# Kernel tuning notes

Hardware: AMD Instinct MI355X
Metric: run time of the kernel (lower is better)

Reference implementation:

```python
import jax, jax.numpy as jnp
import numpy as np

TY = 10  # decoder loop uses the global Ty=10 in the original code


def _bi_lstm_dir(X, Wih, Whh, b, n_hidden):
    # X: (m, T, F); returns hidden states (m, T, n_hidden). Gate order: i,f,g,o.
    m = X.shape[0]
    def step(carry, x_t):
        h, c = carry
        g = x_t @ Wih.T + h @ Whh.T + b
        i, f, gg, o = jnp.split(g, 4, axis=-1)
        c = jax.nn.sigmoid(f) * c + jax.nn.sigmoid(i) * jnp.tanh(gg)
        h = jax.nn.sigmoid(o) * jnp.tanh(c)
        return (h, c), h
    h0 = jnp.zeros((m, n_hidden), X.dtype)
    _, hs = jax.lax.scan(step, (h0, h0), jnp.swapaxes(X, 0, 1))
    return jnp.swapaxes(hs, 0, 1)


def setup_inputs() -> dict:
    key = jax.random.key(0)
    ks = jax.random.split(key, 17)
    m, Tx, F = 256, 256, 128
    n_a, n_s, vocab, attn_h = 256, 512, 1024, 10
    def w(k, shape, fan_in):
        return (jax.random.normal(k, shape, jnp.float32) / np.sqrt(fan_in)).astype(jnp.float32)
    return {
        "X": jax.random.normal(ks[0], (m, Tx, F), jnp.float32),
        "Wih_f": w(ks[1], (4 * n_a, F), F),
        "Whh_f": w(ks[2], (4 * n_a, n_a), n_a),
        "b_f": w(ks[3], (4 * n_a,), n_a),
        "Wih_b": w(ks[4], (4 * n_a, F), F),
        "Whh_b": w(ks[5], (4 * n_a, n_a), n_a),
        "b_b": w(ks[6], (4 * n_a,), n_a),
        "W1": w(ks[7], (attn_h, 2 * n_a + n_s), 2 * n_a + n_s),
        "b1": w(ks[8], (attn_h,), attn_h),
        "W2": w(ks[9], (1, attn_h), attn_h),
        "b2": w(ks[10], (1,), attn_h),
        "Wc_ih": w(ks[11], (4 * n_s, n_s), n_s),
        "Wc_hh": w(ks[12], (4 * n_s, n_s), n_s),
        "bc": w(ks[13], (4 * n_s,), n_s),
        "Wfc": w(ks[14], (vocab, n_s), n_s),
        "bfc": w(ks[15], (vocab,), n_s),
    }


def reference(X, Wih_f, Whh_f, b_f, Wih_b, Whh_b, b_b, W1, b1, W2, b2, Wc_ih, Wc_hh, bc, Wfc, bfc):
    m, Tx, _ = X.shape
    n_a = Whh_f.shape[1]
    n_s = Wc_hh.shape[1]
    # bidirectional encoder
    a_f = _bi_lstm_dir(X, Wih_f, Whh_f, b_f, n_a)
    a_b = _bi_lstm_dir(X[:, ::-1], Wih_b, Whh_b, b_b, n_a)[:, ::-1]
    a = jnp.concatenate([a_f, a_b], axis=-1)  # (m, Tx, 2*n_a)
    # decoder: initial h_n = zeros(m, 2, n_a).flatten(1) == zeros(m, n_s) since n_s = 2*n_a
    s = jnp.zeros((m, n_s), X.dtype)
    c = jnp.zeros((m, n_s), X.dtype)
    outs = []
    for _ in range(TY):
        sp = jnp.broadcast_to(s[:, None, :], (m, Tx, n_s))
        concat = jnp.concatenate([a, sp], axis=-1)           # (m, Tx, 2*n_a + n_s)
        e = jnp.tanh(concat @ W1.T + b1)                     # (m, Tx, 10)
        scores = jax.nn.relu(e @ W2.T + b2)                  # (m, Tx, 1)
        alphas = jax.nn.softmax(scores, axis=1)              # softmax over Tx
        context = jnp.sum(alphas * a, axis=1)                # (m, 2*n_a) == (m, n_s)
        g = context @ Wc_ih.T + s @ Wc_hh.T + bc             # LSTMCell
        i, f, gg, o = jnp.split(g, 4, axis=-1)
        c = jax.nn.sigmoid(f) * c + jax.nn.sigmoid(i) * jnp.tanh(gg)
        s = jax.nn.sigmoid(o) * jnp.tanh(c)
        outs.append(s @ Wfc.T + bfc)                         # (m, vocab)
    return jnp.stack(outs, axis=1)                           # (m, Ty, vocab)
```

## Files before the change

kernel.cpp:

```cpp
#include <hip/hip_runtime.h>
#include <hip/hip_bf16.h>

#define TXN 256
#define NA 256
#define NF 128
#define NS 512
#define TYN 10
#define VOCAB 1024

#define A_STR 392
#define W_STR 392
#define WL_OFF (64 * W_STR)
#define AH_OFF (2 * 64 * W_STR)
#define AL_OFF (AH_OFF + 32 * A_STR)
#define PRE_OFF_US (AL_OFF + 32 * A_STR)
#define ENC_LDS_BYTES (150528 + 32 * 68 * 4 + 64 * 4)

#define D_STR 264
#define D_WH 0
#define D_WL (64 * D_STR)
#define D_AH (2 * 64 * D_STR)
#define D_AL (D_AH + 32 * D_STR)
#define D_PRE_US (D_AL + 32 * D_STR)
#define DEC_LDS_BYTES (101376 + 32 * 68 * 4 + 64 * 4)

typedef __attribute__((ext_vector_type(8))) short bf16x8;
typedef __attribute__((ext_vector_type(4))) float f32x4;

__device__ __forceinline__ float fsigmoid(float x) { return 1.f / (1.f + __expf(-x)); }
__device__ __forceinline__ float ftanh(float x)    { return 1.f - 2.f / (1.f + __expf(2.f * x)); }

__device__ __forceinline__ void split_bf16(float v, unsigned short& hi, unsigned short& lo) {
    __hip_bfloat16 h = __float2bfloat16(v);
    float rem = v - __bfloat162float(h);
    __hip_bfloat16 l = __float2bfloat16(rem);
    hi = *reinterpret_cast<unsigned short*>(&h);
    lo = *reinterpret_cast<unsigned short*>(&l);
}

__device__ __forceinline__ float agent_ld(const float* p) {
    return __hip_atomic_load(p, __ATOMIC_RELAXED, __HIP_MEMORY_SCOPE_AGENT);
}
__device__ __forceinline__ void agent_st(float* p, float v) {
    __hip_atomic_store(p, v, __ATOMIC_RELAXED, __HIP_MEMORY_SCOPE_AGENT);
}
__device__ __forceinline__ unsigned flag_ld(const unsigned* p) {
    return __hip_atomic_load(p, __ATOMIC_RELAXED, __HIP_MEMORY_SCOPE_AGENT);
}
__device__ __forceinline__ void flag_st(unsigned* p, unsigned v) {
    __hip_atomic_store(p, v, __ATOMIC_RELAXED, __HIP_MEMORY_SCOPE_AGENT);
}

__global__ __launch_bounds__(512, 1) void encoder_kernel(
    const float* __restrict__ X,
    const float* __restrict__ Wih_f, const float* __restrict__ Whh_f, const float* __restrict__ b_f,
    const float* __restrict__ Wih_b, const float* __restrict__ Whh_b, const float* __restrict__ b_b,
    float* __restrict__ a, unsigned int* __restrict__ bar)
{
    extern __shared__ unsigned char smem_raw[];
    unsigned short* Wh  = (unsigned short*)smem_raw;
    unsigned short* Wl  = (unsigned short*)smem_raw + WL_OFF;
    unsigned short* Ahh = (unsigned short*)smem_raw + AH_OFF;
    unsigned short* All = (unsigned short*)smem_raw + AL_OFF;
    float* Pre = (float*)(smem_raw + (size_t)PRE_OFF_US * 2);
    float* bsh = Pre + 32 * 68;

    const int tid = threadIdx.x;
    const int xcd = blockIdx.x & 7;
    const int sub = (blockIdx.x >> 3) & 1;
    const int jb  = blockIdx.x >> 4;
    const int dir = sub;
    const int ig  = xcd;
    const int i0 = ig * 32;
    const int j0 = jb * 16;
    const int grp = dir * 8 + ig;
    const int myjb = jb;
    unsigned int* slots = bar + grp * 16;

    const float* __restrict__ Wih = dir ? Wih_b : Wih_f;
    const float* __restrict__ Whh = dir ? Whh_b : Whh_f;
    const float* __restrict__ bv  = dir ? b_b  : b_f;

    if (tid < 64) bsh[tid] = bv[(tid >> 4) * NA + j0 + (tid & 15)];

    {
        const int col = tid & 255;
        const int r0w = (tid >> 8) * 32;
        for (int r = r0w; r < r0w + 32; ++r) {
            int row = (r >> 4) * NA + j0 + (r & 15);
            unsigned short hi, lo;
            split_bf16(Whh[(size_t)row * NA + col], hi, lo);
            Wh[r * W_STR + col] = hi;
            Wl[r * W_STR + col] = lo;
            if (col < NF) {
                split_bf16(Wih[(size_t)row * NF + col], hi, lo);
                Wh[r * W_STR + 256 + col] = hi;
                Wl[r * W_STR + 256 + col] = lo;
            }
        }
    }

    {
        const int col = tid & 255;
        const int r0z = (tid >> 8) * 16;
        #pragma unroll 4
        for (int r = r0z; r < r0z + 16; ++r) {
            Ahh[r * A_STR + col] = 0;
            All[r * A_STR + col] = 0;
        }
    }

    {
        const int t0 = dir ? (TXN - 1) : 0;
        const int kx = tid & 127;
        const int rbase = tid >> 7;
        #pragma unroll 4
        for (int rr = 0; rr < 8; ++rr) {
            int r = rr * 4 + rbase;
            float v = X[((size_t)(i0 + r) * TXN + t0) * NF + kx];
            unsigned short hi, lo;
            split_bf16(v, hi, lo);
            Ahh[r * A_STR + 256 + kx] = hi;
            All[r * A_STR + 256 + kx] = lo;
        }
    }
    __syncthreads();

    float cC = 0.f;
    const int jl  = tid & 15;
    const int epr = tid >> 4;

    const int lane = tid & 63;
    const int wv   = tid >> 6;
    const int rt   = wv >> 1;
    const int g0   = (wv & 1) * 2;
    const int ln   = lane & 15;
    const int quad = lane >> 4;
    const unsigned short* pAh = Ahh + (rt * 16 + ln) * A_STR + quad * 8;
    const unsigned short* pAl = All + (rt * 16 + ln) * A_STR + quad * 8;
    const unsigned short* pW0h = Wh + (g0 * 16 + ln) * W_STR + quad * 8;
    const unsigned short* pW0l = Wl + (g0 * 16 + ln) * W_STR + quad * 8;
    const unsigned short* pW1h = pW0h + 16 * W_STR;
    const unsigned short* pW1l = pW0l + 16 * W_STR;

    for (int step = 0; step < TXN; ++step) {
        const int t = dir ? (TXN - 1 - step) : step;

        f32x4 a0e = {0.f,0.f,0.f,0.f}, a0o = {0.f,0.f,0.f,0.f};
        f32x4 a1e = {0.f,0.f,0.f,0.f}, a1o = {0.f,0.f,0.f,0.f};

        if (tid < 256) {
            #pragma unroll
            for (int k4 = 0; k4 < 4; ++k4) {
                const int kc = 8 + k4;
                bf16x8 fah = *(const bf16x8*)(pAh + kc * 32);
                bf16x8 fal = *(const bf16x8*)(pAl + kc * 32);
                bf16x8 w0h = *(const bf16x8*)(pW0h + kc * 32);
                bf16x8 w0l = *(const bf16x8*)(pW0l + kc * 32);
                bf16x8 w1h = *(const bf16x8*)(pW1h + kc * 32);
                bf16x8 w1l = *(const bf16x8*)(pW1l + kc * 32);
                if ((kc & 1) == 0) {
                    a0e = __builtin_amdgcn_mfma_f32_16x16x32_bf16(fal, w0h, a0e, 0, 0, 0);
                    a0e = __builtin_amdgcn_mfma_f32_16x16x32_bf16(fah, w0l, a0e, 0, 0, 0);
                    a0e = __builtin_amdgcn_mfma_f32_16x16x32_bf16(fah, w0h, a0e, 0, 0, 0);
                    a1e = __builtin_amdgcn_mfma_f32_16x16x32_bf16(fal, w1h, a1e, 0, 0, 0);
                    a1e = __builtin_amdgcn_mfma_f32_16x16x32_bf16(fah, w1l, a1e, 0, 0, 0);
                    a1e = __builtin_amdgcn_mfma_f32_16x16x32_bf16(fah, w1h, a1e, 0, 0, 0);
                } else {
                    a0o = __builtin_amdgcn_mfma_f32_16x16x32_bf16(fal, w0h, a0o, 0, 0, 0);
                    a0o = __builtin_amdgcn_mfma_f32_16x16x32_bf16(fah, w0l, a0o, 0, 0, 0);
                    a0o = __builtin_amdgcn_mfma_f32_16x16x32_bf16(fah, w0h, a0o, 0, 0, 0);
                    a1o = __builtin_amdgcn_mfma_f32_16x16x32_bf16(fal, w1h, a1o, 0, 0, 0);
                    a1o = __builtin_amdgcn_mfma_f32_16x16x32_bf16(fah, w1l, a1o, 0, 0, 0);
                    a1o = __builtin_amdgcn_mfma_f32_16x16x32_bf16(fah, w1h, a1o, 0, 0, 0);
                }
            }
        } else if (step != 0) {
            const int tprev = dir ? (t + 1) : (t - 1);
            const int colh = tid & 255;
            const int jw = colh >> 4;
            while (flag_ld(&slots[jw]) < (unsigned)step) {}
            float hv[32];
            #pragma unroll
            for (int r = 0; r < 32; ++r) {
                hv[r] = agent_ld(&a[(((size_t)(i0 + r) * TXN + tprev) << 9) + dir * NA + colh]);
            }
            #pragma unroll
            for (int r = 0; r < 32; ++r) {
                unsigned short hi, lo;
                split_bf16(hv[r], hi, lo);
                Ahh[r * A_STR + colh] = hi;
                All[r * A_STR + colh] = lo;
            }
        }
        __syncthreads();

        if (tid < 256) {
            #pragma unroll
            for (int kp = 0; kp < 4; ++kp) {
                {
                    const int kc = kp * 2;
                    bf16x8 fah = *(const bf16x8*)(pAh + kc * 32);
                    bf16x8 fal = *(const bf16x8*)(pAl + kc * 32);
                    bf16x8 w0h = *(const bf16x8*)(pW0h + kc * 32);
                    bf16x8 w0l = *(const bf16x8*)(pW0l + kc * 32);
                    bf16x8 w1h = *(const bf16x8*)(pW1h + kc * 32);
                    bf16x8 w1l = *(const bf16x8*)(pW1l + kc * 32);
                    a0e = __builtin_amdgcn_mfma_f32_16x16x32_bf16(fal, w0h, a0e, 0, 0, 0);
                    a0e = __builtin_amdgcn_mfma_f32_16x16x32_bf16(fah, w0l, a0e, 0, 0, 0);
                    a0e = __builtin_amdgcn_mfma_f32_16x16x32_bf16(fah, w0h, a0e, 0, 0, 0);
                    a1e = __builtin_amdgcn_mfma_f32_16x16x32_bf16(fal, w1h, a1e, 0, 0, 0);
                    a1e = __builtin_amdgcn_mfma_f32_16x16x32_bf16(fah, w1l, a1e, 0, 0, 0);
                    a1e = __builtin_amdgcn_mfma_f32_16x16x32_bf16(fah, w1h, a1e, 0, 0, 0);
                }
                {
                    const int kc = kp * 2 + 1;
                    bf16x8 fah = *(const bf16x8*)(pAh + kc * 32);
                    bf16x8 fal = *(const bf16x8*)(pAl + kc * 32);
                    bf16x8 w0h = *(const bf16x8*)(pW0h + kc * 32);
                    bf16x8 w0l = *(const bf16x8*)(pW0l + kc * 32);
                    bf16x8 w1h = *(const bf16x8*)(pW1h + kc * 32);
                    bf16x8 w1l = *(const bf16x8*)(pW1l + kc * 32);
                    a0o = __builtin_amdgcn_mfma_f32_16x16x32_bf16(fal, w0h, a0o, 0, 0, 0);
                    a0o = __builtin_amdgcn_mfma_f32_16x16x32_bf16(fah, w0l, a0o, 0, 0, 0);
                    a0o = __builtin_amdgcn_mfma_f32_16x16x32_bf16(fah, w0h, a0o, 0, 0, 0);
                    a1o = __builtin_amdgcn_mfma_f32_16x16x32_bf16(fal, w1h, a1o, 0, 0, 0);
                    a1o = __builtin_amdgcn_mfma_f32_16x16x32_bf16(fah, w1l, a1o, 0, 0, 0);
                    a1o = __builtin_amdgcn_mfma_f32_16x16x32_bf16(fah, w1h, a1o, 0, 0, 0);
                }
            }
            #pragma unroll
            for (int reg = 0; reg < 4; ++reg) {
                int prow = rt * 16 + quad * 4 + reg;
                Pre[prow * 68 + g0 * 16 + ln]       = a0e[reg] + a0o[reg];
                Pre[prow * 68 + (g0 + 1) * 16 + ln] = a1e[reg] + a1o[reg];
            }
        }
        __syncthreads();

        {
            float gi = fsigmoid(Pre[epr * 68 +      jl] + bsh[jl]);
            float gf = fsigmoid(Pre[epr * 68 + 16 + jl] + bsh[16 + jl]);
            float gg = ftanh  (Pre[epr * 68 + 32 + jl] + bsh[32 + jl]);
            float go = fsigmoid(Pre[epr * 68 + 48 + jl] + bsh[48 + jl]);
            cC = gf * cC + gi * gg;
            float h = go * ftanh(cC);
            agent_st(&a[(((size_t)(i0 + epr) * TXN + t) << 9) + dir * NA + j0 + jl], h);
        }

        if (step != TXN - 1) {
            __syncthreads();
            if (tid == 0) flag_st(&slots[myjb], (unsigned)(step + 1));
            {
                const int tn = dir ? (t - 1) : (t + 1);
                const int kx = tid & 127;
                const int rbase = tid >> 7;
                #pragma unroll 4
                for (int rr = 0; rr < 8; ++rr) {
                    int r = rr * 4 + rbase;
                    float v = X[((size_t)(i0 + r) * TXN + tn) * NF + kx];
                    unsigned short hi, lo;
                    split_bf16(v, hi, lo);
                    Ahh[r * A_STR + 256 + kx] = hi;
                    All[r * A_STR + 256 + kx] = lo;
                }
            }
            __syncthreads();
        }
    }
}

__global__ __launch_bounds__(256) void wsplit_cat(
    const float* __restrict__ Wc_ih, const float* __restrict__ Wc_hh,
    unsigned short* __restrict__ Wh, unsigned short* __restrict__ Wl)
{
    int idx = blockIdx.x * 256 + threadIdx.x;
    int r = idx >> 10, k = idx & 1023;
    float v = (k < 512) ? Wc_ih[(size_t)r * 512 + k] : Wc_hh[(size_t)r * 512 + (k - 512)];
    unsigned short hi, lo;
    split_bf16(v, hi, lo);
    Wh[idx] = hi; Wl[idx] = lo;
}

__global__ __launch_bounds__(256) void wsplit_fc(
    const float* __restrict__ Wfc,
    unsigned short* __restrict__ Wh, unsigned short* __restrict__ Wl)
{
    int idx = blockIdx.x * 256 + threadIdx.x;
    unsigned short hi, lo;
    split_bf16(Wfc[idx], hi, lo);
    Wh[idx] = hi; Wl[idx] = lo;
}

__global__ __launch_bounds__(256) void attn_prep(
    const float* __restrict__ a, const float* __restrict__ W1,
    const float* __restrict__ b1, float* __restrict__ aW1)
{
    __shared__ float Wsh[10][516];
    __shared__ float red[64][10][4];
    const int tid = threadIdx.x;
    for (int idx = tid; idx < 10 * 512; idx += 256) {
        int o = idx >> 9, k = idx & 511;
        Wsh[o][k] = W1[o * 1024 + k];
    }
    __syncthreads();
    const int r = tid >> 2, kq = tid & 3;
    const float* ar = a + ((size_t)blockIdx.x * 64 + r) * 512 + kq * 128;
    float acc[10] = {};
    for (int k = 0; k < 128; k += 4) {
        float4 v = *(const float4*)&ar[k];
        #pragma unroll
        for (int o = 0; o < 10; ++o) {
            float4 w = *(const float4*)&Wsh[o][kq * 128 + k];
            acc[o] += v.x * w.x + v.y * w.y + v.z * w.z + v.w * w.w;
        }
    }
    #pragma unroll
    for (int o = 0; o < 10; ++o) red[r][o][kq] = acc[o];
    __syncthreads();
    for (int idx = tid; idx < 640; idx += 256) {
        int rr = idx / 10, o = idx % 10;
        float s = red[rr][o][0] + red[rr][o][1] + red[rr][o][2] + red[rr][o][3] + b1[o];
        aW1[((size_t)blockIdx.x * 64 + rr) * 10 + o] = s;
    }
}

__global__ __launch_bounds__(256) void attn_kernel(
    const float* __restrict__ aW1,
    const float* __restrict__ s_prev, int sp_stride,
    const float* __restrict__ W1,
    const float* __restrict__ W2,
    const float* __restrict__ b2,
    const float* __restrict__ a,
    float* __restrict__ xcat)
{
    __shared__ float sh_s[10];
    __shared__ float sh_w2[10];
    __shared__ float sred[160];
    __shared__ float red[256];
    __shared__ float al[256];
    __shared__ float4 ctxred[256];
    const int i = blockIdx.x;
    const int tid = threadIdx.x;

    if (tid < 160) {
        int o = tid >> 4, part = tid & 15;
        const float* srow = s_prev + (size_t)i * sp_stride;
        const float* wrow = W1 + o * 1024 + 512;
        float p = 0.f;
        for (int k = part; k < 512; k += 16) p += srow[k] * wrow[k];
        sred[tid] = p;
    }
    __syncthreads();
    if (tid < 10) {
        float v = 0.f;
        #pragma unroll
        for (int p = 0; p < 16; ++p) v += sred[tid * 16 + p];
        sh_s[tid] = v;
        sh_w2[tid] = W2[tid];
    }
    __syncthreads();

    float sum = b2[0];
    const float* ar = aW1 + ((size_t)i * TXN + tid) * 10;
    #pragma unroll
    for (int h = 0; h < 10; ++h) {
        float e = ftanh(ar[h] + sh_s[h]);
        sum += e * sh_w2[h];
    }
    float sc = fmaxf(sum, 0.f);

    red[tid] = sc;
    __syncthreads();
    for (int s = 128; s > 0; s >>= 1) {
        if (tid < s) red[tid] = fmaxf(red[tid], red[tid + s]);
        __syncthreads();
    }
    float mx = red[0];
    __syncthreads();
    float p = __expf(sc - mx);
    red[tid] = p;
    __syncthreads();
    for (int s = 128; s > 0; s >>= 1) {
        if (tid < s) red[tid] += red[tid + s];
        __syncthreads();
    }
    float inv = 1.f / red[0];
    al[tid] = p * inv;
    __syncthreads();

    const int half = tid >> 7;
    const int q    = tid & 127;
    const float* abase = a + (size_t)i * TXN * NS + q * 4;
    float4 acc = make_float4(0.f, 0.f, 0.f, 0.f);
    #pragma unroll 8
    for (int t = half; t < TXN; t += 2) {
        float w = al[t];
        float4 v = *(const float4*)&abase[(size_t)t * NS];
        acc.x += w * v.x; acc.y += w * v.y; acc.z += w * v.z; acc.w += w * v.w;
    }
    ctxred[tid] = acc;
    __syncthreads();
    if (tid < 128) {
        float4 e = ctxred[tid];
        float4 o = ctxred[tid + 128];
        float4 r4 = make_float4(e.x + o.x, e.y + o.y, e.z + o.z, e.w + o.w);
        *(float4*)&xcat[(size_t)i * 512 + tid * 4] = r4;
    }
}

__global__ __launch_bounds__(256, 1) void gates_kernel(
    const float* __restrict__ xcat,
    const float* __restrict__ s_prev, int sp_stride,
    const unsigned short* __restrict__ Wch,
    const unsigned short* __restrict__ Wcl,
    const float* __restrict__ bc,
    float* __restrict__ c_buf,
    float* __restrict__ s_out, int so_stride)
{
    extern __shared__ unsigned char smem_raw[];
    unsigned short* Wh = (unsigned short*)smem_raw + D_WH;
    unsigned short* Wl = (unsigned short*)smem_raw + D_WL;
    unsigned short* Ah = (unsigned short*)smem_raw + D_AH;
    unsigned short* Al = (unsigned short*)smem_raw + D_AL;
    float* Pre = (float*)(smem_raw + (size_t)D_PRE_US * 2);
    float* bsh = Pre + 32 * 68;

    const int tid = threadIdx.x;
    const int i0 = blockIdx.x * 32;
    const int j0 = blockIdx.y * 16;

    if (tid < 64) bsh[tid] = bc[(tid >> 4) * 512 + j0 + (tid & 15)];

    const int lane = tid & 63;
    const int wv   = tid >> 6;
    const int rt   = wv >> 1;
    const int g0   = (wv & 1) * 2;
    const int ln   = lane & 15;
    const int quad = lane >> 4;
    const unsigned short* pAh = Ah + (rt * 16 + ln) * D_STR + quad * 8;
    const unsigned short* pAl = Al + (rt * 16 + ln) * D_STR + quad * 8;
    const unsigned short* pW0h = Wh + (g0 * 16 + ln) * D_STR + quad * 8;
    const unsigned short* pW0l = Wl + (g0 * 16 + ln) * D_STR + quad * 8;
    const unsigned short* pW1h = pW0h + 16 * D_STR;
    const unsigned short* pW1l = pW0l + 16 * D_STR;

    const int rW = tid >> 2;
    const int qW = (tid & 3) * 64;
    const int rowg = (rW >> 4) * 512 + j0 + (rW & 15);

    f32x4 a0 = {0.f,0.f,0.f,0.f}, a1 = {0.f,0.f,0.f,0.f};

    for (int ch = 0; ch < 4; ++ch) {
        const int kc0 = ch * 256;
        __syncthreads();
        #pragma unroll 8
        for (int r = 0; r < 32; ++r) {
            float v;
            if (ch < 2) v = xcat[(size_t)(i0 + r) * 512 + kc0 + tid];
            else        v = s_prev[(size_t)(i0 + r) * sp_stride + (kc0 - 512) + tid];
            unsigned short hi, lo;
            split_bf16(v, hi, lo);
            Ah[r * D_STR + tid] = hi;
            Al[r * D_STR + tid] = lo;
        }
        {
            const size_t base = (size_t)rowg * 1024 + kc0 + qW;
            #pragma unroll
            for (int i = 0; i < 8; ++i) {
                *(bf16x8*)&Wh[rW * D_STR + qW + i * 8] = *(const bf16x8*)&Wch[base + i * 8];
                *(bf16x8*)&Wl[rW * D_STR + qW + i * 8] = *(const bf16x8*)&Wcl[base + i * 8];
            }
        }
        __syncthreads();
        #pragma unroll
        for (int kc = 0; kc < 8; ++kc) {
            bf16x8 fah = *(const bf16x8*)(pAh + kc * 32);
            bf16x8 fal = *(const bf16x8*)(pAl + kc * 32);
            bf16x8 w0h = *(const bf16x8*)(pW0h + kc * 32);
            bf16x8 w0l = *(const bf16x8*)(pW0l + kc * 32);
            bf16x8 w1h = *(const bf16x8*)(pW1h + kc * 32);
            bf16x8 w1l = *(const bf16x8*)(pW1l + kc * 32);
            a0 = __builtin_amdgcn_mfma_f32_16x16x32_bf16(fal, w0h, a0, 0, 0, 0);
            a0 = __builtin_amdgcn_mfma_f32_16x16x32_bf16(fah, w0l, a0, 0, 0, 0);
            a0 = __builtin_amdgcn_mfma_f32_16x16x32_bf16(fah, w0h, a0, 0, 0, 0);
            a1 = __builtin_amdgcn_mfma_f32_16x16x32_bf16(fal, w1h, a1, 0, 0, 0);
            a1 = __builtin_amdgcn_mfma_f32_16x16x32_bf16(fah, w1l, a1, 0, 0, 0);
            a1 = __builtin_amdgcn_mfma_f32_16x16x32_bf16(fah, w1h, a1, 0, 0, 0);
        }
    }
    __syncthreads();
    #pragma unroll
    for (int reg = 0; reg < 4; ++reg) {
        int prow = rt * 16 + quad * 4 + reg;
        Pre[prow * 68 + g0 * 16 + ln]       = a0[reg];
        Pre[prow * 68 + (g0 + 1) * 16 + ln] = a1[reg];
    }
    __syncthreads();

    const int jl = tid & 15;
    const int iA = (tid >> 4) * 2;
    #pragma unroll
    for (int rr = 0; rr < 2; ++rr) {
        int r = iA + rr;
        float gi = fsigmoid(Pre[r * 68 +      jl] + bsh[jl]);
        float gf = fsigmoid(Pre[r * 68 + 16 + jl] + bsh[16 + jl]);
        float gg = ftanh  (Pre[r * 68 + 32 + jl] + bsh[32 + jl]);
        float go = fsigmoid(Pre[r * 68 + 48 + jl] + bsh[48 + jl]);
        size_t ci = (size_t)(i0 + r) * 512 + j0 + jl;
        float cn = gf * c_buf[ci] + gi * gg;
        c_buf[ci] = cn;
        s_out[(size_t)(i0 + r) * so_stride + j0 + jl] = go * ftanh(cn);
    }
}

__global__ __launch_bounds__(256, 1) void logits_kernel(
    const float* __restrict__ S, int s_stride,
    const unsigned short* __restrict__ Wfh,
    const unsigned short* __restrict__ Wfl,
    const float* __restrict__ bfc,
    float* __restrict__ out, int o_stride, int o_off)
{
    extern __shared__ unsigned char smem_raw[];
    unsigned short* Wh = (unsigned short*)smem_raw + D_WH;
    unsigned short* Wl = (unsigned short*)smem_raw + D_WL;
    unsigned short* Ah = (unsigned short*)smem_raw + D_AH;
    unsigned short* Al = (unsigned short*)smem_raw + D_AL;

    const int tid = threadIdx.x;
    const int i0 = blockIdx.x * 32;
    const int v0 = blockIdx.y * 64;

    const int lane = tid & 63;
    const int wv   = tid >> 6;
    const int rt   = wv >> 1;
    const int ct   = wv & 1;
    const int ln   = lane & 15;
    const int quad = lane >> 4;
    const unsigned short* pAh = Ah + (rt * 16 + ln) * D_STR + quad * 8;
    const unsigned short* pAl = Al + (rt * 16 + ln) * D_STR + quad * 8;
    const unsigned short* pW0h = Wh + (ct * 32 + ln) * D_STR + quad * 8;
    const unsigned short* pW0l = Wl + (ct * 32 + ln) * D_STR + quad * 8;
    const unsigned short* pW1h = pW0h + 16 * D_STR;
    const unsigned short* pW1l = pW0l + 16 * D_STR;

    const int rW = tid >> 2;
    const int qW = (tid & 3) * 64;

    f32x4 a0 = {0.f,0.f,0.f,0.f}, a1 = {0.f,0.f,0.f,0.f};

    for (int ch = 0; ch < 2; ++ch) {
        const int kc0 = ch * 256;
        __syncthreads();
        #pragma unroll 8
        for (int r = 0; r < 32; ++r) {
            float v = S[(size_t)(i0 + r) * s_stride + kc0 + tid];
            unsigned short hi, lo;
            split_bf16(v, hi, lo);
            Ah[r * D_STR + tid] = hi;
            Al[r * D_STR + tid] = lo;
        }
        {
            const size_t base = (size_t)(v0 + rW) * 512 + kc0 + qW;
            #pragma unroll
            for (int i = 0; i < 8; ++i) {
                *(bf16x8*)&Wh[rW * D_STR + qW + i * 8] = *(const bf16x8*)&Wfh[base + i * 8];
                *(bf16x8*)&Wl[rW * D_STR + qW + i * 8] = *(const bf16x8*)&Wfl[base + i * 8];
            }
        }
        __syncthreads();
        #pragma unroll
        for (int kc = 0; kc < 8; ++kc) {
            bf16x8 fah = *(const bf16x8*)(pAh + kc * 32);
            bf16x8 fal = *(const bf16x8*)(pAl + kc * 32);
            bf16x8 w0h = *(const bf16x8*)(pW0h + kc * 32);
            bf16x8 w0l = *(const bf16x8*)(pW0l + kc * 32);
            bf16x8 w1h = *(const bf16x8*)(pW1h + kc * 32);
            bf16x8 w1l = *(const bf16x8*)(pW1l + kc * 32);
            a0 = __builtin_amdgcn_mfma_f32_16x16x32_bf16(fal, w0h, a0, 0, 0, 0);
            a0 = __builtin_amdgcn_mfma_f32_16x16x32_bf16(fah, w0l, a0, 0, 0, 0);
            a0 = __builtin_amdgcn_mfma_f32_16x16x32_bf16(fah, w0h, a0, 0, 0, 0);
            a1 = __builtin_amdgcn_mfma_f32_16x16x32_bf16(fal, w1h, a1, 0, 0, 0);
            a1 = __builtin_amdgcn_mfma_f32_16x16x32_bf16(fah, w1l, a1, 0, 0, 0);
            a1 = __builtin_amdgcn_mfma_f32_16x16x32_bf16(fah, w1h, a1, 0, 0, 0);
        }
    }
    #pragma unroll
    for (int reg = 0; reg < 4; ++reg) {
        int row = i0 + rt * 16 + quad * 4 + reg;
        int col0 = v0 + ct * 32 + ln;
        out[(size_t)row * o_stride + o_off + col0]      = a0[reg] + bfc[col0];
        out[(size_t)row * o_stride + o_off + col0 + 16] = a1[reg] + bfc[col0 + 16];
    }
}

extern "C" void kernel_launch(void* const* d_in, const int* in_sizes, int n_in,
                              void* d_out, int out_size, void* d_ws, size_t ws_size,
                              hipStream_t stream)
{
    const float* X     = (const float*)d_in[0];
    const float* Wih_f = (const float*)d_in[1];
    const float* Whh_f = (const float*)d_in[2];
    const float* b_f   = (const float*)d_in[3];
    const float* Wih_b = (const float*)d_in[4];
    const float* Whh_b = (const float*)d_in[5];
    const float* b_b   = (const float*)d_in[6];
    const float* W1    = (const float*)d_in[7];
    const float* b1    = (const float*)d_in[8];
    const float* W2    = (const float*)d_in[9];
    const float* b2    = (const float*)d_in[10];
    const float* Wc_ih = (const float*)d_in[11];
    const float* Wc_hh = (const float*)d_in[12];
    const float* bc    = (const float*)d_in[13];
    const float* Wfc   = (const float*)d_in[14];
    const float* bfc   = (const float*)d_in[15];
    float* out = (float*)d_out;
    float* ws  = (float*)d_ws;

    float* c_buf = ws;
    float* zbuf  = ws + 131072;
    float* sbufB = ws + 262144;
    float* xcat  = ws + 393216;
    float* a     = ws + 524288;
    float* aW1   = ws + 34078720;
    unsigned short* Wch = (unsigned short*)(ws + 34734080);
    unsigned short* Wcl = (unsigned short*)(ws + 35782656);
    unsigned short* Wfh = (unsigned short*)(ws + 36831232);
    unsigned short* Wfl = (unsigned short*)(ws + 37093376);
    unsigned int* bar   = (unsigned int*)(ws + 37355520);
    float* S_all = ws + 37355776;
    const int deferred = (ws_size >= (size_t)38666496 * sizeof(float)) ? 1 : 0;

    static int attrs_set = 0;
    if (!attrs_set) {
        hipFuncSetAttribute(reinterpret_cast<const void*>(encoder_kernel),
                            hipFuncAttributeMaxDynamicSharedMemorySize, ENC_LDS_BYTES);
        hipFuncSetAttribute(reinterpret_cast<const void*>(gates_kernel),
                            hipFuncAttributeMaxDynamicSharedMemorySize, DEC_LDS_BYTES);
        hipFuncSetAttribute(reinterpret_cast<const void*>(logits_kernel),
                            hipFuncAttributeMaxDynamicSharedMemorySize, DEC_LDS_BYTES);
        attrs_set = 1;
    }

    hipMemsetAsync(c_buf, 0, (size_t)262144 * sizeof(float), stream);
    hipMemsetAsync(bar, 0, 256 * sizeof(unsigned int), stream);

    wsplit_cat<<<8192, 256, 0, stream>>>(Wc_ih, Wc_hh, Wch, Wcl);
    wsplit_fc<<<2048, 256, 0, stream>>>(Wfc, Wfh, Wfl);

    {
        void* args[] = { (void*)&X, (void*)&Wih_f, (void*)&Whh_f, (void*)&b_f,
                         (void*)&Wih_b, (void*)&Whh_b, (void*)&b_b, (void*)&a, (void*)&bar };
        hipLaunchCooperativeKernel(reinterpret_cast<void*>(encoder_kernel),
                                   dim3(256), dim3(512), args, ENC_LDS_BYTES, stream);
    }

    attn_prep<<<1024, 256, 0, stream>>>(a, W1, b1, aW1);

    for (int ty = 0; ty < TYN; ++ty) {
        const float* sprev; int spstr;
        float* sout; int sostr;
        if (ty == 0) { sprev = zbuf; spstr = 512; }
        else if (deferred) { sprev = S_all + (size_t)(ty - 1) * 512; spstr = TYN * 512; }
        else { sprev = (ty & 1) ? sbufB : zbuf; spstr = 512; }
        if (deferred) { sout = S_all + (size_t)ty * 512; sostr = TYN * 512; }
        else { sout = (ty & 1) ? zbuf : sbufB; sostr = 512; }

        attn_kernel<<<256, 256, 0, stream>>>(aW1, sprev, spstr, W1, W2, b2, a, xcat);
        gates_kernel<<<dim3(8, 32), 256, DEC_LDS_BYTES, stream>>>(
            xcat, sprev, spstr, Wch, Wcl, bc, c_buf, sout, sostr);
        if (!deferred) {
            logits_kernel<<<dim3(8, 16), 256, DEC_LDS_BYTES, stream>>>(
                sout, 512, Wfh, Wfl, bfc, out, TYN * VOCAB, ty * VOCAB);
        }
    }
    if (deferred) {
        logits_kernel<<<dim3(80, 16), 256, DEC_LDS_BYTES, stream>>>(
            S_all, 512, Wfh, Wfl, bfc, out, VOCAB, 0);
    }
}
```

Before: 1.936 ms.

## Fuse decoder attention and gate steps into one persistent cooperative kernel

Replaces the per-timestep attn_kernel and gates_kernel launches (20 launches) with a single cooperative decoder kernel of 256 blocks that loops over the 10 decoder steps and uses grid-wide syncs between the attention and gate phases. It is meant to remove kernel launch overhead and inter-kernel gaps on the sequential decoder chain. In exchange it adds grid barrier cost and forces one block per CU via launch bounds, with LDS regions aliased between phases. The old multi-launch path remains only when the workspace is too small for deferred logits.

```diff
diff --git a/kernel.cpp b/kernel.cpp
--- a/kernel.cpp
+++ b/kernel.cpp
@@ -1,5 +1,8 @@
 #include <hip/hip_runtime.h>
 #include <hip/hip_bf16.h>
+#include <hip/hip_cooperative_groups.h>
+
+namespace cg = cooperative_groups;
 
 #define TXN 256
 #define NA 256
@@ -325,6 +328,202 @@
     }
 }
 
+__global__ __launch_bounds__(256, 1) void decoder_kernel(
+    const float* __restrict__ aW1,
+    const float* __restrict__ W1,
+    const float* __restrict__ W2,
+    const float* __restrict__ b2,
+    const float* __restrict__ a,
+    float* __restrict__ xcat,
+    const unsigned short* __restrict__ Wch,
+    const unsigned short* __restrict__ Wcl,
+    const float* __restrict__ bc,
+    float* __restrict__ c_buf,
+    float* __restrict__ S_all,
+    const float* __restrict__ zbuf)
+{
+    extern __shared__ unsigned char smem_raw[];
+    unsigned short* Wh = (unsigned short*)smem_raw + D_WH;
+    unsigned short* Wl = (unsigned short*)smem_raw + D_WL;
+    unsigned short* Ah = (unsigned short*)smem_raw + D_AH;
+    unsigned short* Al = (unsigned short*)smem_raw + D_AL;
+    float* Pre = (float*)(smem_raw + (size_t)D_PRE_US * 2);
+    float* bsh = Pre + 32 * 68;
+    float* al    = (float*)smem_raw;
+    float* red   = al + 256;
+    float* sred  = red + 256;
+    float* sh_s  = sred + 160;
+    float* sh_w2 = sh_s + 10;
+    float4* ctxred = (float4*)(smem_raw + 2816);
+
+    cg::grid_group grid = cg::this_grid();
+    const int tid = threadIdx.x;
+    const int blk = blockIdx.x;
+
+    const int gi0 = (blk & 7) * 32;
+    const int gj0 = (blk >> 3) * 16;
+    if (tid < 64) bsh[tid] = bc[(tid >> 4) * 512 + gj0 + (tid & 15)];
+
+    const int lane = tid & 63;
+    const int wv   = tid >> 6;
+    const int rt   = wv >> 1;
+    const int g0   = (wv & 1) * 2;
+    const int ln   = lane & 15;
+    const int quad = lane >> 4;
+    const unsigned short* pAh = Ah + (rt * 16 + ln) * D_STR + quad * 8;
+    const unsigned short* pAl = Al + (rt * 16 + ln) * D_STR + quad * 8;
+    const unsigned short* pW0h = Wh + (g0 * 16 + ln) * D_STR + quad * 8;
+    const unsigned short* pW0l = Wl + (g0 * 16 + ln) * D_STR + quad * 8;
+    const unsigned short* pW1h = pW0h + 16 * D_STR;
+    const unsigned short* pW1l = pW0l + 16 * D_STR;
+    const int rW = tid >> 2;
+    const int qW = (tid & 3) * 64;
+    const int rowg = (rW >> 4) * 512 + gj0 + (rW & 15);
+
+    for (int ty = 0; ty < TYN; ++ty) {
+        const float* sprev = (ty == 0) ? zbuf : (S_all + (size_t)(ty - 1) * 512);
+        const int spstr    = (ty == 0) ? 512 : (TYN * 512);
+        float* sout        = S_all + (size_t)ty * 512;
+        const int sostr    = TYN * 512;
+
+        {
+            const int i = blk;
+            if (tid < 160) {
+                int o = tid >> 4, part = tid & 15;
+                const float* srow = sprev + (size_t)i * spstr;
+                const float* wrow = W1 + o * 1024 + 512;
+                float p = 0.f;
+                for (int k = part; k < 512; k += 16) p += srow[k] * wrow[k];
+                sred[tid] = p;
+            }
+            __syncthreads();
+            if (tid < 10) {
+                float v = 0.f;
+                #pragma unroll
+                for (int p = 0; p < 16; ++p) v += sred[tid * 16 + p];
+                sh_s[tid] = v;
+                sh_w2[tid] = W2[tid];
+            }
+            __syncthreads();
+
+            float sum = b2[0];
+            const float* ar = aW1 + ((size_t)i * TXN + tid) * 10;
+            #pragma unroll
+            for (int h = 0; h < 10; ++h) {
+                float e = ftanh(ar[h] + sh_s[h]);
+                sum += e * sh_w2[h];
+            }
+            float sc = fmaxf(sum, 0.f);
+
+            red[tid] = sc;
+            __syncthreads();
+            for (int s = 128; s > 0; s >>= 1) {
+                if (tid < s) red[tid] = fmaxf(red[tid], red[tid + s]);
+                __syncthreads();
+            }
+            float mx = red[0];
+            __syncthreads();
+            float p = __expf(sc - mx);
+            red[tid] = p;
+            __syncthreads();
+            for (int s = 128; s > 0; s >>= 1) {
+                if (tid < s) red[tid] += red[tid + s];
+                __syncthreads();
+            }
+            float inv = 1.f / red[0];
+            al[tid] = p * inv;
+            __syncthreads();
+
+            const int half = tid >> 7;
+            const int q    = tid & 127;
+            const float* abase = a + (size_t)i * TXN * NS + q * 4;
+            float4 acc = make_float4(0.f, 0.f, 0.f, 0.f);
+            #pragma unroll 8
+            for (int t = half; t < TXN; t += 2) {
+                float w = al[t];
+                float4 v = *(const float4*)&abase[(size_t)t * NS];
+                acc.x += w * v.x; acc.y += w * v.y; acc.z += w * v.z; acc.w += w * v.w;
+            }
+            ctxred[tid] = acc;
+            __syncthreads();
+            if (tid < 128) {
+                float4 e = ctxred[tid];
+                float4 o = ctxred[tid + 128];
+                float4 r4 = make_float4(e.x + o.x, e.y + o.y, e.z + o.z, e.w + o.w);
+                *(float4*)&xcat[(size_t)i * 512 + tid * 4] = r4;
+            }
+        }
+        grid.sync();
+
+        {
+            f32x4 a0 = {0.f,0.f,0.f,0.f}, a1 = {0.f,0.f,0.f,0.f};
+
+            for (int ch = 0; ch < 4; ++ch) {
+                const int kc0 = ch * 256;
+                __syncthreads();
+                #pragma unroll 8
+                for (int r = 0; r < 32; ++r) {
+                    float v;
+                    if (ch < 2) v = xcat[(size_t)(gi0 + r) * 512 + kc0 + tid];
+                    else        v = sprev[(size_t)(gi0 + r) * spstr + (kc0 - 512) + tid];
+                    unsigned short hi, lo;
+                    split_bf16(v, hi, lo);
+                    Ah[r * D_STR + tid] = hi;
+                    Al[r * D_STR + tid] = lo;
+                }
+                {
+                    const size_t base = (size_t)rowg * 1024 + kc0 + qW;
+                    #pragma unroll
+                    for (int i = 0; i < 8; ++i) {
+                        *(bf16x8*)&Wh[rW * D_STR + qW + i * 8] = *(const bf16x8*)&Wch[base + i * 8];
+                        *(bf16x8*)&Wl[rW * D_STR + qW + i * 8] = *(const bf16x8*)&Wcl[base + i * 8];
+                    }
+                }
+                __syncthreads();
+                #pragma unroll
+                for (int kc = 0; kc < 8; ++kc) {
+                    bf16x8 fah = *(const bf16x8*)(pAh + kc * 32);
+                    bf16x8 fal = *(const bf16x8*)(pAl + kc * 32);
+                    bf16x8 w0h = *(const bf16x8*)(pW0h + kc * 32);
+                    bf16x8 w0l = *(const bf16x8*)(pW0l + kc * 32);
+                    bf16x8 w1h = *(const bf16x8*)(pW1h + kc * 32);
+                    bf16x8 w1l = *(const bf16x8*)(pW1l + kc * 32);
+                    a0 = __builtin_amdgcn_mfma_f32_16x16x32_bf16(fal, w0h, a0, 0, 0, 0);
+                    a0 = __builtin_amdgcn_mfma_f32_16x16x32_bf16(fah, w0l, a0, 0, 0, 0);
+                    a0 = __builtin_amdgcn_mfma_f32_16x16x32_bf16(fah, w0h, a0, 0, 0, 0);
+                    a1 = __builtin_amdgcn_mfma_f32_16x16x32_bf16(fal, w1h, a1, 0, 0, 0);
+                    a1 = __builtin_amdgcn_mfma_f32_16x16x32_bf16(fah, w1l, a1, 0, 0, 0);
+                    a1 = __builtin_amdgcn_mfma_f32_16x16x32_bf16(fah, w1h, a1, 0, 0, 0);
+                }
+            }
+            __syncthreads();
+            #pragma unroll
+            for (int reg = 0; reg < 4; ++reg) {
+                int prow = rt * 16 + quad * 4 + reg;
+                Pre[prow * 68 + g0 * 16 + ln]       = a0[reg];
+                Pre[prow * 68 + (g0 + 1) * 16 + ln] = a1[reg];
+            }
+            __syncthreads();
+
+            const int jl = tid & 15;
+            const int iA = (tid >> 4) * 2;
+            #pragma unroll
+            for (int rr = 0; rr < 2; ++rr) {
+                int r = iA + rr;
+                float gi = fsigmoid(Pre[r * 68 +      jl] + bsh[jl]);
+                float gf = fsigmoid(Pre[r * 68 + 16 + jl] + bsh[16 + jl]);
+                float gg = ftanh  (Pre[r * 68 + 32 + jl] + bsh[32 + jl]);
+                float go = fsigmoid(Pre[r * 68 + 48 + jl] + bsh[48 + jl]);
+                size_t ci = (size_t)(gi0 + r) * 512 + gj0 + jl;
+                float cn = gf * c_buf[ci] + gi * gg;
+                c_buf[ci] = cn;
+                sout[(size_t)(gi0 + r) * sostr + gj0 + jl] = go * ftanh(cn);
+            }
+        }
+        grid.sync();
+    }
+}
+
 __global__ __launch_bounds__(256) void attn_kernel(
     const float* __restrict__ aW1,
     const float* __restrict__ s_prev, int sp_stride,
@@ -635,6 +834,8 @@
     if (!attrs_set) {
         hipFuncSetAttribute(reinterpret_cast<const void*>(encoder_kernel),
                             hipFuncAttributeMaxDynamicSharedMemorySize, ENC_LDS_BYTES);
+        hipFuncSetAttribute(reinterpret_cast<const void*>(decoder_kernel),
+                            hipFuncAttributeMaxDynamicSharedMemorySize, DEC_LDS_BYTES);
         hipFuncSetAttribute(reinterpret_cast<const void*>(gates_kernel),
                             hipFuncAttributeMaxDynamicSharedMemorySize, DEC_LDS_BYTES);
         hipFuncSetAttribute(reinterpret_cast<const void*>(logits_kernel),
@@ -657,25 +858,27 @@
 
     attn_prep<<<1024, 256, 0, stream>>>(a, W1, b1, aW1);
 
-    for (int ty = 0; ty < TYN; ++ty) {
-        const float* sprev; int spstr;
-        float* sout; int sostr;
-        if (ty == 0) { sprev = zbuf; spstr = 512; }
-        else if (deferred) { sprev = S_all + (size_t)(ty - 1) * 512; spstr = TYN * 512; }
-        else { sprev = (ty & 1) ? sbufB : zbuf; spstr = 512; }
-        if (deferred) { sout = S_all + (size_t)ty * 512; sostr = TYN * 512; }
-        else { sout = (ty & 1) ? zbuf : sbufB; sostr = 512; }
-
-        attn_kernel<<<256, 256, 0, stream>>>(aW1, sprev, spstr, W1, W2, b2, a, xcat);
-        gates_kernel<<<dim3(8, 32), 256, DEC_LDS_BYTES, stream>>>(
-            xcat, sprev, spstr, Wch, Wcl, bc, c_buf, sout, sostr);
-        if (!deferred) {
+    if (deferred) {
+        void* args[] = { (void*)&aW1, (void*)&W1, (void*)&W2, (void*)&b2,
+                         (void*)&a, (void*)&xcat, (void*)&Wch, (void*)&Wcl,
+                         (void*)&bc, (void*)&c_buf, (void*)&S_all, (void*)&zbuf };
+        hipLaunchCooperativeKernel(reinterpret_cast<void*>(decoder_kernel),
+                                   dim3(256), dim3(256), args, DEC_LDS_BYTES, stream);
+        logits_kernel<<<dim3(80, 16), 256, DEC_LDS_BYTES, stream>>>(
+            S_all, 512, Wfh, Wfl, bfc, out, VOCAB, 0);
+    } else {
+        for (int ty = 0; ty < TYN; ++ty) {
+            const float* sprev; int spstr;
+            float* sout; int sostr;
+            if (ty == 0) { sprev = zbuf; spstr = 512; }
+            else { sprev = (ty & 1) ? sbufB : zbuf; spstr = 512; }
+            sout = (ty & 1) ? zbuf : sbufB; sostr = 512;
+
+            attn_kernel<<<256, 256, 0, stream>>>(aW1, sprev, spstr, W1, W2, b2, a, xcat);
+            gates_kernel<<<dim3(8, 32), 256, DEC_LDS_BYTES, stream>>>(
+                xcat, sprev, spstr, Wch, Wcl, bc, c_buf, sout, sostr);
             logits_kernel<<<dim3(8, 16), 256, DEC_LDS_BYTES, stream>>>(
                 sout, 512, Wfh, Wfl, bfc, out, TYN * VOCAB, ty * VOCAB);
         }
     }
-    if (deferred) {
-        logits_kernel<<<dim3(80, 16), 256, DEC_LDS_BYTES, stream>>>(
-            S_all, 512, Wfh, Wfl, bfc, out, VOCAB, 0);
-    }
-}
+}
```

Result: slower. 2.334 ms (+20.5%).
